# Performance work log

Hardware: AMD Instinct MI355X
Metric: run time of the kernel (lower is better)

## Reference

```python
import jax, jax.numpy as jnp
import numpy as np

T = 40          # self.T / timestep
T_REDUCE = 32
FAC = T_REDUCE / T - 0.001  # 0.799, threshold used by create_spike_input_cuda


def conv_t(x, w, b, pad):
    # x: (N,C,H,W,T); w: (O,I,3,3). SLAYER/catSNN conv = Conv3d with time-kernel 1,
    # i.e. the same 2D conv applied independently at every timestep.
    out = jax.lax.conv_general_dilated(
        x, w[..., None], window_strides=(1, 1, 1),
        padding=[(pad, pad), (pad, pad), (0, 0)],
        dimension_numbers=("NCHWT", "OIHWT", "NCHWT"))
    return out + b[None, :, None, None, None]


def avgpool2(x):
    # 2x2 spatial average pool per timestep (snn.pool(2))
    N, C, H, W, Tt = x.shape
    return x.reshape(N, C, H // 2, 2, W // 2, 2, Tt).mean(axis=(3, 5))


def get_spikes(x, thr):
    # catCuda.getSpikes: integrate-and-fire over the last (time) axis with
    # soft reset (subtract threshold). thr broadcastable to x[..., 0].
    xT = jnp.moveaxis(x, -1, 0)                      # (T, N, C, H, W)
    thr_b = jnp.broadcast_to(jnp.asarray(thr, x.dtype), xT.shape[1:])
    def step(v, xt):
        v = v + xt
        s = (v >= thr_b).astype(x.dtype)
        return v - s * thr_b, s
    _, s = jax.lax.scan(step, jnp.zeros(xT.shape[1:], x.dtype), xT)
    return jnp.moveaxis(s, 0, -1)


def requant(y):
    # create_spike_input_cuda(sum(y, time)/T, T): stack the time-mean T times
    # and spike-generate with threshold FAC.
    ym = jnp.mean(y, axis=-1)                        # sum over time / T
    yb = jnp.broadcast_to(ym[..., None], ym.shape + (T,))
    return get_spikes(yb, FAC)


def tts(xi, yi, thr):
    # threshold_training_snn: per-channel spiking of xi, requantized copy of yi.
    return get_spikes(xi, thr[None, :, None, None]), requant(yi)


def forward(x, thr1, thr2, thr3, thr4, thr5, thr6, thr7, p1, p2, p3, p4,
            w1, b1, w2, b2, w3, b3, w4, b4, w5, b5, w6, b6, w7, b7, wc, bc):
    c = conv_t(x, w1, b1, 1)
    xs, ys = tts(c, c, thr1)
    xs, ys = tts(conv_t(xs, w2, b2, 1), conv_t(ys, w2, b2, 1), thr2)
    xs, ys = tts(avgpool2(xs), avgpool2(ys), p1)
    xs, ys = tts(conv_t(xs, w3, b3, 1), conv_t(ys, w3, b3, 1), thr3)
    xs, ys = tts(conv_t(xs, w4, b4, 1), conv_t(ys, w4, b4, 1), thr4)
    xs, ys = tts(avgpool2(xs), avgpool2(ys), p2)
    xs, ys = tts(conv_t(xs, w5, b5, 1), conv_t(ys, w5, b5, 1), thr5)
    xs, ys = tts(conv_t(xs, w6, b6, 1), conv_t(ys, w6, b6, 1), thr6)
    xs, ys = tts(avgpool2(xs), avgpool2(ys), p3)
    xs, ys = tts(conv_t(xs, w7, b7, 0), conv_t(ys, w7, b7, 0), thr7)
    xs, ys = tts(avgpool2(xs), avgpool2(ys), p4)
    N = xs.shape[0]
    xr = xs.reshape(N, 1024, T)                      # spatial is 1x1 here
    logits = jnp.einsum("nct,oc->not", xr, wc) + bc[None, :, None]
    out = jnp.sum(logits, axis=-1) / T               # sum_spikes / T
    return out.reshape(N, 10, 1, 1)


def setup_inputs() -> dict:
    key = jax.random.key(0)
    ks = jax.random.split(key, 32)
    inp = {}
    inp["x"] = jax.random.uniform(ks[0], (2, 3, 32, 32, T), jnp.float32)
    chans = [(3, 128), (128, 128), (128, 256), (256, 256),
             (256, 512), (512, 512), (512, 1024)]
    for i, (ci, co) in enumerate(chans, 1):
        inp[f"w{i}"] = jax.random.normal(ks[i], (co, ci, 3, 3), jnp.float32) * (2.0 / (ci * 9)) ** 0.5
        inp[f"b{i}"] = jnp.zeros((co,), jnp.float32)
    inp["wc"] = jax.random.normal(ks[8], (10, 1024), jnp.float32) * 0.03
    inp["bc"] = jnp.zeros((10,), jnp.float32)
    thr_dims = {"thr1": 128, "thr2": 128, "p1": 128, "thr3": 256, "thr4": 256,
                "p2": 256, "thr5": 512, "thr6": 512, "p3": 512, "thr7": 1024, "p4": 1024}
    for j, (name, d) in enumerate(thr_dims.items()):
        inp[name] = 0.2 + jax.random.uniform(ks[9 + j], (d,), jnp.float32)
    return inp


def reference(x, thr1, thr2, thr3, thr4, thr5, thr6, thr7, p1, p2, p3, p4,
              w1, b1, w2, b2, w3, b3, w4, b4, w5, b5, w6, b6, w7, b7, wc, bc):
    return forward(x, thr1, thr2, thr3, thr4, thr5, thr6, thr7, p1, p2, p3, p4,
                   w1, b1, w2, b2, w3, b3, w4, b4, w5, b5, w6, b6, w7, b7, wc, bc)
```

## Files before the change

kernel.cpp:

```cpp
#include <hip/hip_runtime.h>


constexpr int NT = 40;

typedef __attribute__((ext_vector_type(8))) short s16x8;
typedef __attribute__((ext_vector_type(4))) float f32x4;

__device__ __forceinline__ float bf2f(unsigned short u) {
    return __uint_as_float(((unsigned)u) << 16);
}

__device__ __forceinline__ void wg_barrier() {
    __builtin_amdgcn_sched_barrier(0);
    __builtin_amdgcn_s_barrier();
    __builtin_amdgcn_sched_barrier(0);
}

__global__ __launch_bounds__(256) void transpose_w(
    const float* __restrict__ w, float* __restrict__ wt, int CO, int R)
{
    __shared__ float tile[32][33];
    const int r0 = blockIdx.x * 32, c0 = blockIdx.y * 32;
    const int tx = threadIdx.x % 32, ty = threadIdx.x / 32;
#pragma unroll
    for (int k = 0; k < 4; k++) {
        const int co = c0 + ty + k * 8, r = r0 + tx;
        if (co < CO && r < R) tile[ty + k * 8][tx] = w[(size_t)co * R + r];
    }
    __syncthreads();
#pragma unroll
    for (int k = 0; k < 4; k++) {
        const int r = r0 + ty + k * 8, co = c0 + tx;
        if (r < R && co < CO) wt[(size_t)r * CO + co] = tile[tx][ty + k * 8];
    }
}

__global__ __launch_bounds__(320) void conv1_c(
    const float* __restrict__ in, const float* __restrict__ wt,
    const float* __restrict__ bias, float* __restrict__ out)
{
    __shared__ float xs_[27 * NT];
    __shared__ float wl[27 * 128];
    const int sp = blockIdx.x;
    const int ho = sp >> 5, wo = sp & 31;
    const int n = blockIdx.z;
    const int tid = threadIdx.x;
    const int tt = tid >> 5;
    const int cc = tid & 31;

    float4 acc[4];
#pragma unroll
    for (int j = 0; j < 4; j++) {
        const float bv = bias[cc * 4 + j];
        acc[j] = make_float4(bv, bv, bv, bv);
    }
    for (int u = tid; u < 270; u += 320) {
        const int r = u / 10, q = u % 10;
        const int cil = r / 9, k = r % 9;
        const int hi = ho + k / 3 - 1, wi = wo + k % 3 - 1;
        float4 v = make_float4(0.f, 0.f, 0.f, 0.f);
        if ((unsigned)hi < 32u && (unsigned)wi < 32u)
            v = *reinterpret_cast<const float4*>(
                in + ((size_t)((n * 3 + cil) * 1024 + hi * 32 + wi)) * NT + q * 4);
        *reinterpret_cast<float4*>(&xs_[r * NT + q * 4]) = v;
    }
    for (int u = tid; u < 864; u += 320) {
        const int r = u >> 5, j = u & 31;
        *reinterpret_cast<float4*>(&wl[r * 128 + j * 4]) =
            *reinterpret_cast<const float4*>(wt + r * 128 + j * 4);
    }
    __syncthreads();
#pragma unroll
    for (int r = 0; r < 27; ++r) {
        const float4 xv = *reinterpret_cast<const float4*>(&xs_[r * NT + tt * 4]);
        const float4 wv = *reinterpret_cast<const float4*>(&wl[r * 128 + cc * 4]);
        acc[0].x = fmaf(xv.x, wv.x, acc[0].x); acc[0].y = fmaf(xv.y, wv.x, acc[0].y);
        acc[0].z = fmaf(xv.z, wv.x, acc[0].z); acc[0].w = fmaf(xv.w, wv.x, acc[0].w);
        acc[1].x = fmaf(xv.x, wv.y, acc[1].x); acc[1].y = fmaf(xv.y, wv.y, acc[1].y);
        acc[1].z = fmaf(xv.z, wv.y, acc[1].z); acc[1].w = fmaf(xv.w, wv.y, acc[1].w);
        acc[2].x = fmaf(xv.x, wv.z, acc[2].x); acc[2].y = fmaf(xv.y, wv.z, acc[2].y);
        acc[2].z = fmaf(xv.z, wv.z, acc[2].z); acc[2].w = fmaf(xv.w, wv.z, acc[2].w);
        acc[3].x = fmaf(xv.x, wv.w, acc[3].x); acc[3].y = fmaf(xv.y, wv.w, acc[3].y);
        acc[3].z = fmaf(xv.z, wv.w, acc[3].z); acc[3].w = fmaf(xv.w, wv.w, acc[3].w);
    }
    const size_t base = (size_t)(n * 1024 + sp) * (NT * 128);
#pragma unroll
    for (int j = 0; j < 4; j++) {
        const int cb = cc * 4 + j;
        out[base + (tt * 4 + 0) * 128 + cb] = acc[j].x;
        out[base + (tt * 4 + 1) * 128 + cb] = acc[j].y;
        out[base + (tt * 4 + 2) * 128 + cb] = acc[j].z;
        out[base + (tt * 4 + 3) * 128 + cb] = acc[j].w;
    }
}

__global__ void split_w(const float* __restrict__ w,
                        unsigned short* __restrict__ hi, unsigned short* __restrict__ mid,
                        unsigned short* __restrict__ lo, int CO, int CIN_)
{
    const int idx = blockIdx.x * blockDim.x + threadIdx.x;
    if (idx >= CO * CIN_) return;
    const int co = idx / CIN_, ci = idx % CIN_;
    const float* src = w + ((size_t)co * CIN_ + ci) * 9;
#pragma unroll
    for (int k = 0; k < 9; ++k) {
        const float f = src[k];
        const unsigned u = __float_as_uint(f);
        const float fh = __uint_as_float(u & 0xFFFF0000u);
        const float r1 = f - fh;
        const unsigned u1 = __float_as_uint(r1);
        const float fm = __uint_as_float(u1 & 0xFFFF0000u);
        const float r2 = r1 - fm;
        const unsigned u2 = __float_as_uint(r2);
        const size_t dst = ((size_t)k * CO + co) * CIN_ + ci;
        hi[dst] = (unsigned short)(u >> 16);
        mid[dst] = (unsigned short)(u1 >> 16);
        lo[dst] = (unsigned short)(u2 >> 16);
    }
}

template<int CIN_SEG, int COUT, int HP, int WP, int NSPLIT>
__global__ __launch_bounds__(256, 2) void conv_t14(
    const unsigned short* __restrict__ spk,
    const unsigned short* __restrict__ wlo, const unsigned short* __restrict__ wmid,
    const unsigned short* __restrict__ whi,
    const float* __restrict__ bias, float* __restrict__ out)
{
    constexpr int CIN = CIN_SEG * NSPLIT;
    constexpr int HO = HP - 2, WO = WP - 2;
    constexpr int MROW = WO * NT;
    constexpr int MTILES = (MROW + 63) / 64;
    constexpr bool RAGGED = (MROW % 64) != 0;
    constexpr int KC = CIN_SEG / 64;
    constexpr int NCHUNK = 9 * KC;
    static_assert(NCHUNK % 3 == 0, "rotation unrolled by 3");
    constexpr int NX = HO * MTILES;
    constexpr int NY = COUT / 64;
    constexpr int NB = NX * NY * NSPLIT;
    static_assert(NB % 8 == 0, "grid must divide across 8 XCDs");
    constexpr int Q = NB / 8;
    constexpr size_t SLAB = (size_t)2 * HO * WO * NT * COUT;

    __shared__ unsigned short smem[20480];

    const int g = blockIdx.x;
    const int orig = (g & 7) * Q + (g >> 3);
    const int x = orig % NX;
    const int y = (orig / NX) % NY;
    const int split = orig / (NX * NY);
    const int ho = x / MTILES;
    const int m0 = (x % MTILES) * 64;
    const int co0 = y * 64;

    const int tid = threadIdx.x;
    const int lane = tid & 63;
    const int wv = tid >> 6;
    const int wm = wv >> 1, wn = wv & 1;
    const int lr = lane >> 4, lc = lane & 15;
    const int rlane = lane >> 3, blane = lane & 7;
    const int swz = ((blane ^ rlane) << 3);

    int lofs[10]; int arow[10]; int gstat[10]; const unsigned short* wbase[10]; bool isA[10];
#pragma unroll
    for (int s = 0; s < 10; ++s) {
        const int slot = wv * 10 + s;
        if (slot < 16) {
            const int img = slot >> 3, r0 = (slot & 7) << 3;
            isA[s] = true;
            arow[s] = m0 + r0 + rlane;
            lofs[s] = (img * 64 + r0 + rlane) * 64 + swz;
            gstat[s] = (int)((img * HP * WP * NT + arow[s]) * CIN + blane * 8);
            wbase[s] = spk;
        } else {
            const int si = slot - 16;
            const int sp_ = si >> 3, r0 = (si & 7) << 3;
            isA[s] = false;
            arow[s] = 0;
            lofs[s] = 8192 + (sp_ * 64 + r0 + rlane) * 64 + swz;
            gstat[s] = (int)((co0 + r0 + rlane) * CIN + blane * 8);
            wbase[s] = (sp_ == 0) ? wlo : ((sp_ == 1) ? wmid : whi);
        }
    }

    f32x4 acc[2][2][2];
#pragma unroll
    for (int img = 0; img < 2; ++img)
#pragma unroll
        for (int mf = 0; mf < 2; ++mf)
#pragma unroll
            for (int nf = 0; nf < 2; ++nf) {
                const float bv = (NSPLIT == 1 || split == 0)
                    ? bias[co0 + wn * 32 + nf * 16 + lc] : 0.f;
                acc[img][mf][nf] = {bv, bv, bv, bv};
            }

    auto loadchunk = [&](s16x8 (&r)[10], int c) {
        const int kh = c / (3 * KC);
        const int rem = c - kh * 3 * KC;
        const int kw = rem / KC;
        const int kc = rem - kw * KC;
        const int khw = kh * 3 + kw;
        const int ci0 = split * CIN_SEG + kc * 64;
        const size_t aoff = ((size_t)(ho + kh) * WP * NT + (size_t)kw * NT) * CIN + ci0;
        const size_t boff = (size_t)khw * COUT * CIN + ci0;
#pragma unroll
        for (int s = 0; s < 10; ++s) {
            if (isA[s]) {
                if (!RAGGED) {
                    r[s] = *(const s16x8*)(spk + aoff + (size_t)gstat[s]);
                } else {
                    s16x8 v = {0, 0, 0, 0, 0, 0, 0, 0};
                    if (arow[s] < MROW)
                        v = *(const s16x8*)(spk + aoff + (size_t)gstat[s]);
                    r[s] = v;
                }
            } else {
                r[s] = *(const s16x8*)(wbase[s] + boff + (size_t)gstat[s]);
            }
        }
    };

    auto writechunk = [&](s16x8 (&r)[10]) {
#pragma unroll
        for (int s = 0; s < 10; ++s)
            *(s16x8*)&smem[lofs[s]] = r[s];
    };

    auto compute = [&]() {
        __builtin_amdgcn_s_setprio(1);
#pragma unroll
        for (int kcs = 0; kcs < 2; ++kcs) {
            const int cswz = (((kcs * 4 + lr) ^ (lc & 7)) << 3);
            s16x8 af[2][2];
#pragma unroll
            for (int img = 0; img < 2; ++img)
#pragma unroll
                for (int mf = 0; mf < 2; ++mf)
                    af[img][mf] = *(const s16x8*)&smem[(img * 64 + wm * 32 + mf * 16 + lc) * 64 + cswz];
#pragma unroll
            for (int s = 0; s < 3; ++s)
#pragma unroll
                for (int nf = 0; nf < 2; ++nf) {
                    const s16x8 bq = *(const s16x8*)&smem[8192 + s * 4096 + (wn * 32 + nf * 16 + lc) * 64 + cswz];
#pragma unroll
                    for (int img = 0; img < 2; ++img)
#pragma unroll
                        for (int mf = 0; mf < 2; ++mf)
                            acc[img][mf][nf] = __builtin_amdgcn_mfma_f32_16x16x32_bf16(
                                af[img][mf], bq, acc[img][mf][nf], 0, 0, 0);
                }
        }
        __builtin_amdgcn_s_setprio(0);
    };

    s16x8 ra[10], rb[10], rc[10];
    loadchunk(ra, 0);
    loadchunk(rb, 1);
#pragma unroll 1
    for (int c = 0; c < NCHUNK; c += 3) {
        writechunk(ra);
        if (c + 2 < NCHUNK) loadchunk(rc, c + 2);
        asm volatile("s_waitcnt lgkmcnt(0)" ::: "memory");
        wg_barrier();
        compute();
        wg_barrier();
        writechunk(rb);
        if (c + 3 < NCHUNK) loadchunk(ra, c + 3);
        asm volatile("s_waitcnt lgkmcnt(0)" ::: "memory");
        wg_barrier();
        compute();
        wg_barrier();
        writechunk(rc);
        if (c + 4 < NCHUNK) loadchunk(rb, c + 4);
        asm volatile("s_waitcnt lgkmcnt(0)" ::: "memory");
        wg_barrier();
        compute();
        wg_barrier();
    }

#pragma unroll
    for (int img = 0; img < 2; ++img) {
        float* outp = out + (size_t)split * SLAB + ((size_t)(img * HO + ho) * WO * NT) * COUT;
#pragma unroll
        for (int mf = 0; mf < 2; ++mf) {
            const int mbase = m0 + wm * 32 + mf * 16;
            if (RAGGED && mbase >= MROW) continue;
#pragma unroll
            for (int nf = 0; nf < 2; ++nf) {
                const int col = co0 + wn * 32 + nf * 16 + lc;
#pragma unroll
                for (int j = 0; j < 4; ++j) {
                    const int m = mbase + lr * 4 + j;
                    outp[(size_t)m * COUT + col] = acc[img][mf][nf][j];
                }
            }
        }
    }
}

__global__ void if_ci(const float* __restrict__ in, unsigned short* __restrict__ spk,
                      const float* __restrict__ thr, int C, int HO, int WO,
                      int HP, int WP, int off, int total, int nslab, size_t slab,
                      int nmain, int halocells)
{
    if ((int)blockIdx.x >= nmain) {
        const int hb = blockIdx.x - nmain;
        const int n = hb / halocells, cell = hb % halocells;
        int h, w;
        if (cell < WP)          { h = 0;      w = cell; }
        else if (cell < 2 * WP) { h = HP - 1; w = cell - WP; }
        else { const int s = cell - 2 * WP; h = 1 + (s >> 1); w = (s & 1) ? (WP - 1) : 0; }
        unsigned short* p = spk + (((size_t)(n * HP + h) * WP) + w) * (size_t)(NT * C);
        const s16x8 z = {0, 0, 0, 0, 0, 0, 0, 0};
        for (int i = threadIdx.x * 8; i < NT * C; i += blockDim.x * 8)
            *(s16x8*)(p + i) = z;
        return;
    }
    const int idx = blockIdx.x * blockDim.x + threadIdx.x;
    if (idx >= total) return;
    const int c = idx % C;
    const int sp = idx / C;
    const int wo = sp % WO;
    const int ho = (sp / WO) % HO;
    const int n = sp / (WO * HO);
    const float th = thr[c];
    const size_t ib = (size_t)sp * NT * C + c;
    const size_t ob = (((size_t)(n * HP + ho + off) * WP) + wo + off) * NT * C + c;
    float v = 0.f;
#pragma unroll 1
    for (int t = 0; t < NT; ++t) {
        float x = 0.f;
        for (int s = 0; s < nslab; ++s) x += in[ib + (size_t)s * slab + (size_t)t * C];
        v += x;
        const float s = (v >= th) ? 1.f : 0.f;
        v -= s * th;
        spk[ob + (size_t)t * C] = (s != 0.f) ? (unsigned short)0x3F80 : (unsigned short)0;
    }
}

__global__ void pool_ci(const unsigned short* __restrict__ in, unsigned short* __restrict__ out,
                        const float* __restrict__ thr, int C, int HO, int WO,
                        int IHP, int IWP, int offi, int OHP, int OWP, int offo,
                        int total, int nmain, int halocells)
{
    if ((int)blockIdx.x >= nmain) {
        const int hb = blockIdx.x - nmain;
        const int n = hb / halocells, cell = hb % halocells;
        int h, w;
        if (cell < OWP)          { h = 0;       w = cell; }
        else if (cell < 2 * OWP) { h = OHP - 1; w = cell - OWP; }
        else { const int s = cell - 2 * OWP; h = 1 + (s >> 1); w = (s & 1) ? (OWP - 1) : 0; }
        unsigned short* p = out + (((size_t)(n * OHP + h) * OWP) + w) * (size_t)(NT * C);
        const s16x8 z = {0, 0, 0, 0, 0, 0, 0, 0};
        for (int i = threadIdx.x * 8; i < NT * C; i += blockDim.x * 8)
            *(s16x8*)(p + i) = z;
        return;
    }
    const int idx = blockIdx.x * blockDim.x + threadIdx.x;
    if (idx >= total) return;
    const int c = idx % C;
    const int sp = idx / C;
    const int wo = sp % WO;
    const int ho = (sp / WO) % HO;
    const int n = sp / (WO * HO);
    const float th = thr[c];
    const size_t i00 = (((size_t)(n * IHP + 2 * ho + offi) * IWP) + 2 * wo + offi) * NT * C + c;
    const size_t dW = (size_t)NT * C, dH = (size_t)IWP * NT * C;
    const size_t ob = (((size_t)(n * OHP + ho + offo) * OWP) + wo + offo) * NT * C + c;
    float v = 0.f;
#pragma unroll
    for (int t = 0; t < NT; ++t) {
        const size_t o = (size_t)t * C;
        const float a = bf2f(in[i00 + o]) + bf2f(in[i00 + dW + o]) +
                        bf2f(in[i00 + dH + o]) + bf2f(in[i00 + dH + dW + o]);
        v += a * 0.25f;
        const float s = (v >= th) ? 1.f : 0.f;
        v -= s * th;
        out[ob + o] = (s != 0.f) ? (unsigned short)0x3F80 : (unsigned short)0;
    }
}

__global__ __launch_bounds__(1024) void classifier_ci(
    const unsigned short* __restrict__ s, const float* __restrict__ wc,
    const float* __restrict__ bc, float* __restrict__ out)
{
    __shared__ float cnt[2][1024];
    const int c = threadIdx.x;
    for (int n = 0; n < 2; n++) {
        float sum = 0.f;
#pragma unroll
        for (int t = 0; t < NT; ++t) sum += bf2f(s[(size_t)(n * NT + t) * 1024 + c]);
        cnt[n][c] = sum;
    }
    __syncthreads();
    if (threadIdx.x < 20) {
        const int n = threadIdx.x / 10, o = threadIdx.x % 10;
        float a = 0.f;
        for (int k = 0; k < 1024; k++) a += cnt[n][k] * wc[o * 1024 + k];
        out[n * 10 + o] = a * (1.f / 40.f) + bc[o];
    }
}

extern "C" void kernel_launch(void* const* d_in, const int* in_sizes, int n_in,
                              void* d_out, int out_size, void* d_ws, size_t ws_size,
                              hipStream_t stream)
{
    const float* x   = (const float*)d_in[0];
    const float* w1  = (const float*)d_in[1];  const float* b1 = (const float*)d_in[2];
    const float* w2  = (const float*)d_in[3];  const float* b2 = (const float*)d_in[4];
    const float* w3  = (const float*)d_in[5];  const float* b3 = (const float*)d_in[6];
    const float* w4  = (const float*)d_in[7];  const float* b4 = (const float*)d_in[8];
    const float* w5  = (const float*)d_in[9];  const float* b5 = (const float*)d_in[10];
    const float* w6  = (const float*)d_in[11]; const float* b6 = (const float*)d_in[12];
    const float* w7  = (const float*)d_in[13]; const float* b7 = (const float*)d_in[14];
    const float* wc  = (const float*)d_in[15]; const float* bc = (const float*)d_in[16];
    const float* thr1 = (const float*)d_in[17];
    const float* thr2 = (const float*)d_in[18];
    const float* p1   = (const float*)d_in[19];
    const float* thr3 = (const float*)d_in[20];
    const float* thr4 = (const float*)d_in[21];
    const float* p2   = (const float*)d_in[22];
    const float* thr5 = (const float*)d_in[23];
    const float* thr6 = (const float*)d_in[24];
    const float* p3   = (const float*)d_in[25];
    const float* thr7 = (const float*)d_in[26];
    const float* p4   = (const float*)d_in[27];

    char* W0 = (char*)d_ws;
    float* OUT = (float*)W0;
    unsigned short* WH   = (unsigned short*)(W0 + (44ull << 20));
    unsigned short* WMID = (unsigned short*)(W0 + (53ull << 20));
    unsigned short* WLO  = (unsigned short*)(W0 + (62ull << 20));
    unsigned short* R1   = (unsigned short*)(W0 + (71ull << 20));
    unsigned short* R2   = (unsigned short*)(W0 + (95ull << 20));
    unsigned short* R3   = (unsigned short*)(W0 + (102ull << 20));
    float* WT1 = (float*)(W0 + (122ull << 20));
    unsigned short* S1 = R1, *S3 = R1, *S5 = R1;
    unsigned short* S2 = R2, *S4 = R2, *S6 = R2;
    unsigned short* U2 = R3, *U4 = R3, *U6 = R3;
    unsigned short* S7 = R3;
    unsigned short* P4 = (unsigned short*)((char*)R3 + (2ull << 20));
    float* O = (float*)d_out;

    transpose_w<<<dim3(1, 4), 256, 0, stream>>>(w1, WT1, 128, 27);
    conv1_c<<<dim3(1024, 1, 2), 320, 0, stream>>>(x, WT1, b1, OUT);
    if_ci<<<1024 + 264, 256, 0, stream>>>(OUT, S1, thr1, 128, 32, 32, 34, 34, 1,
                                          262144, 1, 0, 1024, 132);

    split_w<<<64, 256, 0, stream>>>(w2, WH, WMID, WLO, 128, 128);
    conv_t14<128, 128, 34, 34, 1><<<1280, 256, 0, stream>>>(S1, WLO, WMID, WH, b2, OUT);
    if_ci<<<1024, 256, 0, stream>>>(OUT, U2, thr2, 128, 32, 32, 32, 32, 0,
                                    262144, 1, 0, 1024, 0);
    pool_ci<<<256 + 136, 256, 0, stream>>>(U2, S2, p1, 128, 16, 16, 32, 32, 0,
                                           18, 18, 1, 65536, 256, 68);

    split_w<<<128, 256, 0, stream>>>(w3, WH, WMID, WLO, 256, 128);
    conv_t14<128, 256, 18, 18, 1><<<640, 256, 0, stream>>>(S2, WLO, WMID, WH, b3, OUT);
    if_ci<<<512 + 136, 256, 0, stream>>>(OUT, S3, thr3, 256, 16, 16, 18, 18, 1,
                                         131072, 1, 0, 512, 68);

    split_w<<<256, 256, 0, stream>>>(w4, WH, WMID, WLO, 256, 256);
    conv_t14<256, 256, 18, 18, 1><<<640, 256, 0, stream>>>(S3, WLO, WMID, WH, b4, OUT);
    if_ci<<<512, 256, 0, stream>>>(OUT, U4, thr4, 256, 16, 16, 16, 16, 0,
                                   131072, 1, 0, 512, 0);
    pool_ci<<<128 + 72, 256, 0, stream>>>(U4, S4, p2, 256, 8, 8, 16, 16, 0,
                                          10, 10, 1, 32768, 128, 36);

    split_w<<<512, 256, 0, stream>>>(w5, WH, WMID, WLO, 512, 256);
    conv_t14<128, 512, 10, 10, 2><<<640, 256, 0, stream>>>(S4, WLO, WMID, WH, b5, OUT);
    if_ci<<<256 + 72, 256, 0, stream>>>(OUT, S5, thr5, 512, 8, 8, 10, 10, 1,
                                        65536, 2, 2621440, 256, 36);

    split_w<<<1024, 256, 0, stream>>>(w6, WH, WMID, WLO, 512, 512);
    conv_t14<256, 512, 10, 10, 2><<<640, 256, 0, stream>>>(S5, WLO, WMID, WH, b6, OUT);
    if_ci<<<256, 256, 0, stream>>>(OUT, U6, thr6, 512, 8, 8, 8, 8, 0,
                                   65536, 2, 2621440, 256, 0);
    pool_ci<<<64, 256, 0, stream>>>(U6, S6, p3, 512, 4, 4, 8, 8, 0, 4, 4, 0,
                                    16384, 64, 0);

    split_w<<<2048, 256, 0, stream>>>(w7, WH, WMID, WLO, 1024, 512);
    conv_t14<64, 1024, 4, 4, 8><<<512, 256, 0, stream>>>(S6, WLO, WMID, WH, b7, OUT);
    if_ci<<<32, 256, 0, stream>>>(OUT, S7, thr7, 1024, 2, 2, 2, 2, 0,
                                  8192, 8, 327680, 32, 0);
    pool_ci<<<8, 256, 0, stream>>>(S7, P4, p4, 1024, 1, 1, 2, 2, 0, 1, 1, 0,
                                   2048, 8, 0);

    classifier_ci<<<1, 1024, 0, stream>>>(P4, wc, bc, O);
}
```

Baseline: 659.7 us.

## Load conv A operands directly to registers and double-buffer weight tiles in LDS

The conv kernel stops staging activation (A) tiles through shared memory. Each wave now loads its MFMA A fragments straight from global memory into registers, and only the three weight split tiles go through LDS, which is double-buffered so there is one barrier per chunk instead of two. The integrate-and-fire kernel is templated on the slab count and prefetches all timesteps into registers before the serial scan. The trade-off is higher register pressure and A fragments that are loaded redundantly across waves sharing the same rows.

```diff
diff --git a/kernel.cpp b/kernel.cpp
--- a/kernel.cpp
+++ b/kernel.cpp
@@ -120,7 +120,7 @@
 }
 
 template<int CIN_SEG, int COUT, int HP, int WP, int NSPLIT>
-__global__ __launch_bounds__(256, 2) void conv_t14(
+__global__ __launch_bounds__(256, 2) void conv_v3(
     const unsigned short* __restrict__ spk,
     const unsigned short* __restrict__ wlo, const unsigned short* __restrict__ wmid,
     const unsigned short* __restrict__ whi,
@@ -133,7 +133,6 @@
     constexpr bool RAGGED = (MROW % 64) != 0;
     constexpr int KC = CIN_SEG / 64;
     constexpr int NCHUNK = 9 * KC;
-    static_assert(NCHUNK % 3 == 0, "rotation unrolled by 3");
     constexpr int NX = HO * MTILES;
     constexpr int NY = COUT / 64;
     constexpr int NB = NX * NY * NSPLIT;
@@ -141,7 +140,7 @@
     constexpr int Q = NB / 8;
     constexpr size_t SLAB = (size_t)2 * HO * WO * NT * COUT;
 
-    __shared__ unsigned short smem[20480];
+    __shared__ unsigned short smem[2][12288];
 
     const int g = blockIdx.x;
     const int orig = (g & 7) * Q + (g >> 3);
@@ -158,29 +157,27 @@
     const int wm = wv >> 1, wn = wv & 1;
     const int lr = lane >> 4, lc = lane & 15;
     const int rlane = lane >> 3, blane = lane & 7;
-    const int swz = ((blane ^ rlane) << 3);
-
-    int lofs[10]; int arow[10]; int gstat[10]; const unsigned short* wbase[10]; bool isA[10];
-#pragma unroll
-    for (int s = 0; s < 10; ++s) {
-        const int slot = wv * 10 + s;
-        if (slot < 16) {
-            const int img = slot >> 3, r0 = (slot & 7) << 3;
-            isA[s] = true;
-            arow[s] = m0 + r0 + rlane;
-            lofs[s] = (img * 64 + r0 + rlane) * 64 + swz;
-            gstat[s] = (int)((img * HP * WP * NT + arow[s]) * CIN + blane * 8);
-            wbase[s] = spk;
-        } else {
-            const int si = slot - 16;
-            const int sp_ = si >> 3, r0 = (si & 7) << 3;
-            isA[s] = false;
-            arow[s] = 0;
-            lofs[s] = 8192 + (sp_ * 64 + r0 + rlane) * 64 + swz;
-            gstat[s] = (int)((co0 + r0 + rlane) * CIN + blane * 8);
-            wbase[s] = (sp_ == 0) ? wlo : ((sp_ == 1) ? wmid : whi);
-        }
-    }
+
+    int lofs[6]; int bofl[6]; const unsigned short* wbase[6];
+#pragma unroll
+    for (int s = 0; s < 6; ++s) {
+        const int slot = wv * 6 + s;
+        const int sp_ = slot >> 3, r0 = (slot & 7) << 3;
+        const int row = r0 + rlane;
+        lofs[s] = (sp_ * 64 + row) * 64 + ((blane ^ (row & 7)) << 3);
+        bofl[s] = (co0 + row) * CIN + blane * 8;
+        wbase[s] = (sp_ == 0) ? wlo : ((sp_ == 1) ? wmid : whi);
+    }
+
+    int abase[2][2]; bool aok[2];
+#pragma unroll
+    for (int img = 0; img < 2; ++img)
+#pragma unroll
+        for (int mf = 0; mf < 2; ++mf)
+            abase[img][mf] = (img * HP * WP * NT + m0 + wm * 32 + mf * 16 + lc) * CIN + lr * 8;
+#pragma unroll
+    for (int mf = 0; mf < 2; ++mf)
+        aok[mf] = (m0 + wm * 32 + mf * 16 + lc) < MROW;
 
     f32x4 acc[2][2][2];
 #pragma unroll
@@ -194,87 +191,96 @@
                 acc[img][mf][nf] = {bv, bv, bv, bv};
             }
 
-    auto loadchunk = [&](s16x8 (&r)[10], int c) {
+    auto loadB = [&](s16x8 (&r)[6], int c) {
         const int kh = c / (3 * KC);
         const int rem = c - kh * 3 * KC;
         const int kw = rem / KC;
         const int kc = rem - kw * KC;
-        const int khw = kh * 3 + kw;
-        const int ci0 = split * CIN_SEG + kc * 64;
-        const size_t aoff = ((size_t)(ho + kh) * WP * NT + (size_t)kw * NT) * CIN + ci0;
-        const size_t boff = (size_t)khw * COUT * CIN + ci0;
-#pragma unroll
-        for (int s = 0; s < 10; ++s) {
-            if (isA[s]) {
-                if (!RAGGED) {
-                    r[s] = *(const s16x8*)(spk + aoff + (size_t)gstat[s]);
-                } else {
-                    s16x8 v = {0, 0, 0, 0, 0, 0, 0, 0};
-                    if (arow[s] < MROW)
-                        v = *(const s16x8*)(spk + aoff + (size_t)gstat[s]);
-                    r[s] = v;
+        const size_t boff = (size_t)((kh * 3 + kw) * COUT) * CIN + split * CIN_SEG + kc * 64;
+#pragma unroll
+        for (int s = 0; s < 6; ++s)
+            r[s] = *(const s16x8*)(wbase[s] + boff + (size_t)bofl[s]);
+    };
+
+    auto loadA = [&](s16x8 (&a)[2][2][2], int c) {
+        const int kh = c / (3 * KC);
+        const int rem = c - kh * 3 * KC;
+        const int kw = rem / KC;
+        const int kc = rem - kw * KC;
+        const size_t aoff = ((size_t)(ho + kh) * WP * NT + (size_t)kw * NT) * CIN
+                            + split * CIN_SEG + kc * 64;
+#pragma unroll
+        for (int kcs = 0; kcs < 2; ++kcs)
+#pragma unroll
+            for (int img = 0; img < 2; ++img)
+#pragma unroll
+                for (int mf = 0; mf < 2; ++mf) {
+                    s16x8 v = *(const s16x8*)(spk + aoff + (size_t)abase[img][mf] + kcs * 32);
+                    if (RAGGED) {
+                        const s16x8 z = {0, 0, 0, 0, 0, 0, 0, 0};
+                        v = aok[mf] ? v : z;
+                    }
+                    a[kcs][img][mf] = v;
                 }
-            } else {
-                r[s] = *(const s16x8*)(wbase[s] + boff + (size_t)gstat[s]);
-            }
-        }
     };
 
-    auto writechunk = [&](s16x8 (&r)[10]) {
-#pragma unroll
-        for (int s = 0; s < 10; ++s)
-            *(s16x8*)&smem[lofs[s]] = r[s];
+    auto wrB = [&](s16x8 (&r)[6], int buf) {
+#pragma unroll
+        for (int s = 0; s < 6; ++s)
+            *(s16x8*)&smem[buf][lofs[s]] = r[s];
     };
 
-    auto compute = [&]() {
+    auto compute = [&](const unsigned short* sb, s16x8 (&a)[2][2][2]) {
         __builtin_amdgcn_s_setprio(1);
 #pragma unroll
         for (int kcs = 0; kcs < 2; ++kcs) {
-            const int cswz = (((kcs * 4 + lr) ^ (lc & 7)) << 3);
-            s16x8 af[2][2];
-#pragma unroll
-            for (int img = 0; img < 2; ++img)
-#pragma unroll
-                for (int mf = 0; mf < 2; ++mf)
-                    af[img][mf] = *(const s16x8*)&smem[(img * 64 + wm * 32 + mf * 16 + lc) * 64 + cswz];
 #pragma unroll
             for (int s = 0; s < 3; ++s)
 #pragma unroll
                 for (int nf = 0; nf < 2; ++nf) {
-                    const s16x8 bq = *(const s16x8*)&smem[8192 + s * 4096 + (wn * 32 + nf * 16 + lc) * 64 + cswz];
+                    const int row = wn * 32 + nf * 16 + lc;
+                    const s16x8 bq = *(const s16x8*)&sb[(s * 64 + row) * 64
+                                        + (((kcs * 4 + lr) ^ (row & 7)) << 3)];
 #pragma unroll
                     for (int img = 0; img < 2; ++img)
 #pragma unroll
                         for (int mf = 0; mf < 2; ++mf)
                             acc[img][mf][nf] = __builtin_amdgcn_mfma_f32_16x16x32_bf16(
-                                af[img][mf], bq, acc[img][mf][nf], 0, 0, 0);
+                                a[kcs][img][mf], bq, acc[img][mf][nf], 0, 0, 0);
                 }
         }
         __builtin_amdgcn_s_setprio(0);
     };
 
-    s16x8 ra[10], rb[10], rc[10];
-    loadchunk(ra, 0);
-    loadchunk(rb, 1);
+    s16x8 rA[6], rB[6];
+    s16x8 aE[2][2][2], aO[2][2][2];
+    loadB(rA, 0);
+    wrB(rA, 0);
+    loadB(rA, 1);
+    loadB(rB, 2);
+    loadA(aE, 0);
+    asm volatile("s_waitcnt lgkmcnt(0)" ::: "memory");
+    wg_barrier();
 #pragma unroll 1
-    for (int c = 0; c < NCHUNK; c += 3) {
-        writechunk(ra);
-        if (c + 2 < NCHUNK) loadchunk(rc, c + 2);
+    for (int c = 0; c < NCHUNK; c += 2) {
+        if (c + 1 < NCHUNK) {
+            wrB(rA, 1);
+            loadA(aO, c + 1);
+        }
+        if (c + 3 < NCHUNK) loadB(rA, c + 3);
+        __builtin_amdgcn_sched_barrier(0);
+        compute(smem[0], aE);
         asm volatile("s_waitcnt lgkmcnt(0)" ::: "memory");
         wg_barrier();
-        compute();
-        wg_barrier();
-        writechunk(rb);
-        if (c + 3 < NCHUNK) loadchunk(ra, c + 3);
+        if (c + 1 >= NCHUNK) break;
+        if (c + 2 < NCHUNK) {
+            wrB(rB, 0);
+            loadA(aE, c + 2);
+        }
+        if (c + 4 < NCHUNK) loadB(rB, c + 4);
+        __builtin_amdgcn_sched_barrier(0);
+        compute(smem[1], aO);
         asm volatile("s_waitcnt lgkmcnt(0)" ::: "memory");
-        wg_barrier();
-        compute();
-        wg_barrier();
-        writechunk(rc);
-        if (c + 4 < NCHUNK) loadchunk(rb, c + 4);
-        asm volatile("s_waitcnt lgkmcnt(0)" ::: "memory");
-        wg_barrier();
-        compute();
         wg_barrier();
     }
 
@@ -298,9 +304,10 @@
     }
 }
 
+template<int NSLAB>
 __global__ void if_ci(const float* __restrict__ in, unsigned short* __restrict__ spk,
                       const float* __restrict__ thr, int C, int HO, int WO,
-                      int HP, int WP, int off, int total, int nslab, size_t slab,
+                      int HP, int WP, int off, int total, size_t slab,
                       int nmain, int halocells)
 {
     if ((int)blockIdx.x >= nmain) {
@@ -326,12 +333,18 @@
     const float th = thr[c];
     const size_t ib = (size_t)sp * NT * C + c;
     const size_t ob = (((size_t)(n * HP + ho + off) * WP) + wo + off) * NT * C + c;
+    float xs[NT];
+#pragma unroll
+    for (int t = 0; t < NT; ++t) {
+        float x = in[ib + (size_t)t * C];
+#pragma unroll
+        for (int s = 1; s < NSLAB; ++s) x += in[ib + (size_t)s * slab + (size_t)t * C];
+        xs[t] = x;
+    }
     float v = 0.f;
-#pragma unroll 1
+#pragma unroll
     for (int t = 0; t < NT; ++t) {
-        float x = 0.f;
-        for (int s = 0; s < nslab; ++s) x += in[ib + (size_t)s * slab + (size_t)t * C];
-        v += x;
+        v += xs[t];
         const float s = (v >= th) ? 1.f : 0.f;
         v -= s * th;
         spk[ob + (size_t)t * C] = (s != 0.f) ? (unsigned short)0x3F80 : (unsigned short)0;
@@ -444,44 +457,44 @@
 
     transpose_w<<<dim3(1, 4), 256, 0, stream>>>(w1, WT1, 128, 27);
     conv1_c<<<dim3(1024, 1, 2), 320, 0, stream>>>(x, WT1, b1, OUT);
-    if_ci<<<1024 + 264, 256, 0, stream>>>(OUT, S1, thr1, 128, 32, 32, 34, 34, 1,
-                                          262144, 1, 0, 1024, 132);
+    if_ci<1><<<1024 + 264, 256, 0, stream>>>(OUT, S1, thr1, 128, 32, 32, 34, 34, 1,
+                                             262144, 0, 1024, 132);
 
     split_w<<<64, 256, 0, stream>>>(w2, WH, WMID, WLO, 128, 128);
-    conv_t14<128, 128, 34, 34, 1><<<1280, 256, 0, stream>>>(S1, WLO, WMID, WH, b2, OUT);
-    if_ci<<<1024, 256, 0, stream>>>(OUT, U2, thr2, 128, 32, 32, 32, 32, 0,
-                                    262144, 1, 0, 1024, 0);
+    conv_v3<128, 128, 34, 34, 1><<<1280, 256, 0, stream>>>(S1, WLO, WMID, WH, b2, OUT);
+    if_ci<1><<<1024, 256, 0, stream>>>(OUT, U2, thr2, 128, 32, 32, 32, 32, 0,
+                                       262144, 0, 1024, 0);
     pool_ci<<<256 + 136, 256, 0, stream>>>(U2, S2, p1, 128, 16, 16, 32, 32, 0,
                                            18, 18, 1, 65536, 256, 68);
 
     split_w<<<128, 256, 0, stream>>>(w3, WH, WMID, WLO, 256, 128);
-    conv_t14<128, 256, 18, 18, 1><<<640, 256, 0, stream>>>(S2, WLO, WMID, WH, b3, OUT);
-    if_ci<<<512 + 136, 256, 0, stream>>>(OUT, S3, thr3, 256, 16, 16, 18, 18, 1,
-                                         131072, 1, 0, 512, 68);
+    conv_v3<128, 256, 18, 18, 1><<<640, 256, 0, stream>>>(S2, WLO, WMID, WH, b3, OUT);
+    if_ci<1><<<512 + 136, 256, 0, stream>>>(OUT, S3, thr3, 256, 16, 16, 18, 18, 1,
+                                            131072, 0, 512, 68);
 
     split_w<<<256, 256, 0, stream>>>(w4, WH, WMID, WLO, 256, 256);
-    conv_t14<256, 256, 18, 18, 1><<<640, 256, 0, stream>>>(S3, WLO, WMID, WH, b4, OUT);
-    if_ci<<<512, 256, 0, stream>>>(OUT, U4, thr4, 256, 16, 16, 16, 16, 0,
-                                   131072, 1, 0, 512, 0);
+    conv_v3<256, 256, 18, 18, 1><<<640, 256, 0, stream>>>(S3, WLO, WMID, WH, b4, OUT);
+    if_ci<1><<<512, 256, 0, stream>>>(OUT, U4, thr4, 256, 16, 16, 16, 16, 0,
+                                      131072, 0, 512, 0);
     pool_ci<<<128 + 72, 256, 0, stream>>>(U4, S4, p2, 256, 8, 8, 16, 16, 0,
                                           10, 10, 1, 32768, 128, 36);
 
     split_w<<<512, 256, 0, stream>>>(w5, WH, WMID, WLO, 512, 256);
-    conv_t14<128, 512, 10, 10, 2><<<640, 256, 0, stream>>>(S4, WLO, WMID, WH, b5, OUT);
-    if_ci<<<256 + 72, 256, 0, stream>>>(OUT, S5, thr5, 512, 8, 8, 10, 10, 1,
-                                        65536, 2, 2621440, 256, 36);
+    conv_v3<128, 512, 10, 10, 2><<<640, 256, 0, stream>>>(S4, WLO, WMID, WH, b5, OUT);
+    if_ci<2><<<256 + 72, 256, 0, stream>>>(OUT, S5, thr5, 512, 8, 8, 10, 10, 1,
+                                           65536, 2621440, 256, 36);
 
     split_w<<<1024, 256, 0, stream>>>(w6, WH, WMID, WLO, 512, 512);
-    conv_t14<256, 512, 10, 10, 2><<<640, 256, 0, stream>>>(S5, WLO, WMID, WH, b6, OUT);
-    if_ci<<<256, 256, 0, stream>>>(OUT, U6, thr6, 512, 8, 8, 8, 8, 0,
-                                   65536, 2, 2621440, 256, 0);
+    conv_v3<256, 512, 10, 10, 2><<<640, 256, 0, stream>>>(S5, WLO, WMID, WH, b6, OUT);
+    if_ci<2><<<256, 256, 0, stream>>>(OUT, U6, thr6, 512, 8, 8, 8, 8, 0,
+                                      65536, 2621440, 256, 0);
     pool_ci<<<64, 256, 0, stream>>>(U6, S6, p3, 512, 4, 4, 8, 8, 0, 4, 4, 0,
                                     16384, 64, 0);
 
     split_w<<<2048, 256, 0, stream>>>(w7, WH, WMID, WLO, 1024, 512);
-    conv_t14<64, 1024, 4, 4, 8><<<512, 256, 0, stream>>>(S6, WLO, WMID, WH, b7, OUT);
-    if_ci<<<32, 256, 0, stream>>>(OUT, S7, thr7, 1024, 2, 2, 2, 2, 0,
-                                  8192, 8, 327680, 32, 0);
+    conv_v3<64, 1024, 4, 4, 8><<<512, 256, 0, stream>>>(S6, WLO, WMID, WH, b7, OUT);
+    if_ci<8><<<32, 256, 0, stream>>>(OUT, S7, thr7, 1024, 2, 2, 2, 2, 0,
+                                     8192, 327680, 32, 0);
     pool_ci<<<8, 256, 0, stream>>>(S7, P4, p4, 1024, 1, 1, 2, 2, 0, 1, 1, 0,
                                    2048, 8, 0);
 
```

After: 748.0 us. +13.4%, slower.

## Split-K conv layers further, template IF kernel on slab count, raise occupancy

Applied to the files above, without the earlier changes.

Doubles the input-channel split for conv layers 3-6, so each launches twice as many workgroups, each over a smaller K segment. Partial sums go to separate slabs that the IF kernel then adds. The IF kernel is templated on the slab count and loads all 40 timesteps up front into registers, unrolled, which exposes memory parallelism. The conv launch bound is raised from 2 to 4 waves per EU, which may force register spills, and the extra slabs add more partial-sum write and read traffic.

```diff
diff --git a/kernel.cpp b/kernel.cpp
--- a/kernel.cpp
+++ b/kernel.cpp
@@ -120,7 +120,7 @@
 }
 
 template<int CIN_SEG, int COUT, int HP, int WP, int NSPLIT>
-__global__ __launch_bounds__(256, 2) void conv_t14(
+__global__ __launch_bounds__(256, 4) void conv_t14(
     const unsigned short* __restrict__ spk,
     const unsigned short* __restrict__ wlo, const unsigned short* __restrict__ wmid,
     const unsigned short* __restrict__ whi,
@@ -298,9 +298,10 @@
     }
 }
 
+template<int NSLAB>
 __global__ void if_ci(const float* __restrict__ in, unsigned short* __restrict__ spk,
                       const float* __restrict__ thr, int C, int HO, int WO,
-                      int HP, int WP, int off, int total, int nslab, size_t slab,
+                      int HP, int WP, int off, int total, size_t slab,
                       int nmain, int halocells)
 {
     if ((int)blockIdx.x >= nmain) {
@@ -326,12 +327,18 @@
     const float th = thr[c];
     const size_t ib = (size_t)sp * NT * C + c;
     const size_t ob = (((size_t)(n * HP + ho + off) * WP) + wo + off) * NT * C + c;
+    float xs[NT];
+#pragma unroll
+    for (int t = 0; t < NT; ++t) {
+        float x = in[ib + (size_t)t * C];
+#pragma unroll
+        for (int s = 1; s < NSLAB; ++s) x += in[ib + (size_t)s * slab + (size_t)t * C];
+        xs[t] = x;
+    }
     float v = 0.f;
-#pragma unroll 1
+#pragma unroll
     for (int t = 0; t < NT; ++t) {
-        float x = 0.f;
-        for (int s = 0; s < nslab; ++s) x += in[ib + (size_t)s * slab + (size_t)t * C];
-        v += x;
+        v += xs[t];
         const float s = (v >= th) ? 1.f : 0.f;
         v -= s * th;
         spk[ob + (size_t)t * C] = (s != 0.f) ? (unsigned short)0x3F80 : (unsigned short)0;
@@ -444,44 +451,44 @@
 
     transpose_w<<<dim3(1, 4), 256, 0, stream>>>(w1, WT1, 128, 27);
     conv1_c<<<dim3(1024, 1, 2), 320, 0, stream>>>(x, WT1, b1, OUT);
-    if_ci<<<1024 + 264, 256, 0, stream>>>(OUT, S1, thr1, 128, 32, 32, 34, 34, 1,
-                                          262144, 1, 0, 1024, 132);
+    if_ci<1><<<1024 + 264, 256, 0, stream>>>(OUT, S1, thr1, 128, 32, 32, 34, 34, 1,
+                                             262144, 0, 1024, 132);
 
     split_w<<<64, 256, 0, stream>>>(w2, WH, WMID, WLO, 128, 128);
     conv_t14<128, 128, 34, 34, 1><<<1280, 256, 0, stream>>>(S1, WLO, WMID, WH, b2, OUT);
-    if_ci<<<1024, 256, 0, stream>>>(OUT, U2, thr2, 128, 32, 32, 32, 32, 0,
-                                    262144, 1, 0, 1024, 0);
+    if_ci<1><<<1024, 256, 0, stream>>>(OUT, U2, thr2, 128, 32, 32, 32, 32, 0,
+                                       262144, 0, 1024, 0);
     pool_ci<<<256 + 136, 256, 0, stream>>>(U2, S2, p1, 128, 16, 16, 32, 32, 0,
                                            18, 18, 1, 65536, 256, 68);
 
     split_w<<<128, 256, 0, stream>>>(w3, WH, WMID, WLO, 256, 128);
-    conv_t14<128, 256, 18, 18, 1><<<640, 256, 0, stream>>>(S2, WLO, WMID, WH, b3, OUT);
-    if_ci<<<512 + 136, 256, 0, stream>>>(OUT, S3, thr3, 256, 16, 16, 18, 18, 1,
-                                         131072, 1, 0, 512, 68);
+    conv_t14<64, 256, 18, 18, 2><<<1280, 256, 0, stream>>>(S2, WLO, WMID, WH, b3, OUT);
+    if_ci<2><<<512 + 136, 256, 0, stream>>>(OUT, S3, thr3, 256, 16, 16, 18, 18, 1,
+                                            131072, 5242880, 512, 68);
 
     split_w<<<256, 256, 0, stream>>>(w4, WH, WMID, WLO, 256, 256);
-    conv_t14<256, 256, 18, 18, 1><<<640, 256, 0, stream>>>(S3, WLO, WMID, WH, b4, OUT);
-    if_ci<<<512, 256, 0, stream>>>(OUT, U4, thr4, 256, 16, 16, 16, 16, 0,
-                                   131072, 1, 0, 512, 0);
+    conv_t14<128, 256, 18, 18, 2><<<1280, 256, 0, stream>>>(S3, WLO, WMID, WH, b4, OUT);
+    if_ci<2><<<512, 256, 0, stream>>>(OUT, U4, thr4, 256, 16, 16, 16, 16, 0,
+                                      131072, 5242880, 512, 0);
     pool_ci<<<128 + 72, 256, 0, stream>>>(U4, S4, p2, 256, 8, 8, 16, 16, 0,
                                           10, 10, 1, 32768, 128, 36);
 
     split_w<<<512, 256, 0, stream>>>(w5, WH, WMID, WLO, 512, 256);
-    conv_t14<128, 512, 10, 10, 2><<<640, 256, 0, stream>>>(S4, WLO, WMID, WH, b5, OUT);
-    if_ci<<<256 + 72, 256, 0, stream>>>(OUT, S5, thr5, 512, 8, 8, 10, 10, 1,
-                                        65536, 2, 2621440, 256, 36);
+    conv_t14<64, 512, 10, 10, 4><<<1280, 256, 0, stream>>>(S4, WLO, WMID, WH, b5, OUT);
+    if_ci<4><<<256 + 72, 256, 0, stream>>>(OUT, S5, thr5, 512, 8, 8, 10, 10, 1,
+                                           65536, 2621440, 256, 36);
 
     split_w<<<1024, 256, 0, stream>>>(w6, WH, WMID, WLO, 512, 512);
-    conv_t14<256, 512, 10, 10, 2><<<640, 256, 0, stream>>>(S5, WLO, WMID, WH, b6, OUT);
-    if_ci<<<256, 256, 0, stream>>>(OUT, U6, thr6, 512, 8, 8, 8, 8, 0,
-                                   65536, 2, 2621440, 256, 0);
+    conv_t14<128, 512, 10, 10, 4><<<1280, 256, 0, stream>>>(S5, WLO, WMID, WH, b6, OUT);
+    if_ci<4><<<256, 256, 0, stream>>>(OUT, U6, thr6, 512, 8, 8, 8, 8, 0,
+                                      65536, 2621440, 256, 0);
     pool_ci<<<64, 256, 0, stream>>>(U6, S6, p3, 512, 4, 4, 8, 8, 0, 4, 4, 0,
                                     16384, 64, 0);
 
     split_w<<<2048, 256, 0, stream>>>(w7, WH, WMID, WLO, 1024, 512);
     conv_t14<64, 1024, 4, 4, 8><<<512, 256, 0, stream>>>(S6, WLO, WMID, WH, b7, OUT);
-    if_ci<<<32, 256, 0, stream>>>(OUT, S7, thr7, 1024, 2, 2, 2, 2, 0,
-                                  8192, 8, 327680, 32, 0);
+    if_ci<8><<<32, 256, 0, stream>>>(OUT, S7, thr7, 1024, 2, 2, 2, 2, 0,
+                                     8192, 327680, 32, 0);
     pool_ci<<<8, 256, 0, stream>>>(S7, P4, p4, 1024, 1, 1, 2, 2, 0, 1, 1, 0,
                                    2048, 8, 0);
 
```

Result: slower. 2.137 ms (+224.0%).
